# Performance work log

Measured on AMD Instinct MI355X. Metric: run time of the kernel, lower is better.

The kernel has to match this reference:

```python
import jax, jax.numpy as jnp
import numpy as np

RANK = 16
ALPHA = 32
SCALING = ALPHA / RANK  # 2.0


def setup_inputs() -> dict:
    key = jax.random.key(0)
    k1, k2, k3 = jax.random.split(key, 3)
    B_, S, D, O = 2, 4096, 4096, 4096
    x = jax.random.normal(k1, (B_, S, D), dtype=jnp.float32)
    # Dequantized base weight, torch Linear layout [out, in]
    W_base = jax.random.normal(k2, (O, D), dtype=jnp.float32) * 0.02
    # kaiming_uniform-ish init for lora_A [rank, in]
    bound = float(np.sqrt(6.0 / (1 + 5) / D))
    A = jax.random.uniform(k3, (RANK, D), dtype=jnp.float32, minval=-bound, maxval=bound)
    # lora_B initialized to zeros [out, rank]
    Bm = jnp.zeros((O, RANK), dtype=jnp.float32)
    return {"x": x, "W_base": W_base, "A": A, "B": Bm}


def reference(x, W_base, A, B):
    # Y = x @ W_base^T + (x @ A^T) @ B^T * scaling   (dropout p=0 -> identity)
    base_out = jnp.einsum('bsd,od->bso', x, W_base)
    lora_mid = jnp.einsum('bsd,rd->bsr', x, A)        # [B,S,rank]
    lora_out = jnp.einsum('bsr,or->bso', lora_mid, B) # [B,S,out]
    return base_out + lora_out * SCALING
```

## Files before the change

kernel.cpp:

```cpp
#include <hip/hip_runtime.h>
#include <hip/hip_bf16.h>

typedef __attribute__((ext_vector_type(8))) __bf16 bf16x8;
typedef __attribute__((ext_vector_type(4))) float  f32x4;

__global__ __launch_bounds__(256) void cvt_f32_bf16(
    const float* __restrict__ in, __bf16* __restrict__ out, long n8)
{
    long i = (long)blockIdx.x * blockDim.x + threadIdx.x;
    long stride = (long)gridDim.x * blockDim.x;
    for (; i < n8; i += stride) {
        const f32x4* p = (const f32x4*)(in + i * 8);
        f32x4 a = p[0], b = p[1];
        bf16x8 o;
        o[0] = (__bf16)a[0]; o[1] = (__bf16)a[1];
        o[2] = (__bf16)a[2]; o[3] = (__bf16)a[3];
        o[4] = (__bf16)b[0]; o[5] = (__bf16)b[1];
        o[6] = (__bf16)b[2]; o[7] = (__bf16)b[3];
        *(bf16x8*)(out + i * 8) = o;
    }
}

__global__ __launch_bounds__(256) void mid_and_cvt(
    const float* __restrict__ x, const float* __restrict__ A,
    float* __restrict__ mid, __bf16* __restrict__ Xb, int K, int M)
{
    int tid = threadIdx.x;
    int m0 = blockIdx.x * 4;

    float acc[4][16];
#pragma unroll
    for (int row = 0; row < 4; ++row)
#pragma unroll
        for (int r = 0; r < 16; ++r) acc[row][r] = 0.f;

    int iters = K / 2048;
    for (int it = 0; it < iters; ++it) {
        int k = it * 2048 + tid * 8;
        f32x4 xv[4][2];
#pragma unroll
        for (int row = 0; row < 4; ++row) {
            if (m0 + row < M) {
                const float* xr = x + (size_t)(m0 + row) * K;
                xv[row][0] = *(const f32x4*)(xr + k);
                xv[row][1] = *(const f32x4*)(xr + k + 4);
            } else {
                f32x4 z = {0.f,0.f,0.f,0.f};
                xv[row][0] = z; xv[row][1] = z;
            }
            if (Xb && m0 + row < M) {
                bf16x8 o;
                o[0] = (__bf16)xv[row][0][0]; o[1] = (__bf16)xv[row][0][1];
                o[2] = (__bf16)xv[row][0][2]; o[3] = (__bf16)xv[row][0][3];
                o[4] = (__bf16)xv[row][1][0]; o[5] = (__bf16)xv[row][1][1];
                o[6] = (__bf16)xv[row][1][2]; o[7] = (__bf16)xv[row][1][3];
                *(bf16x8*)(Xb + (size_t)(m0 + row) * K + k) = o;
            }
        }
#pragma unroll
        for (int r = 0; r < 16; ++r) {
            const f32x4* ap = (const f32x4*)(A + (size_t)r * K + k);
            f32x4 a0 = ap[0], a1 = ap[1];
#pragma unroll
            for (int row = 0; row < 4; ++row) {
                acc[row][r] += xv[row][0][0]*a0[0] + xv[row][0][1]*a0[1]
                             + xv[row][0][2]*a0[2] + xv[row][0][3]*a0[3]
                             + xv[row][1][0]*a1[0] + xv[row][1][1]*a1[1]
                             + xv[row][1][2]*a1[2] + xv[row][1][3]*a1[3];
            }
        }
    }

#pragma unroll
    for (int row = 0; row < 4; ++row)
#pragma unroll
        for (int r = 0; r < 16; ++r)
#pragma unroll
            for (int off = 32; off > 0; off >>= 1)
                acc[row][r] += __shfl_down(acc[row][r], off, 64);

    __shared__ float red[4][4][16];
    int lane = tid & 63, w = tid >> 6;
    if (lane == 0) {
#pragma unroll
        for (int row = 0; row < 4; ++row)
#pragma unroll
            for (int r = 0; r < 16; ++r) red[w][row][r] = acc[row][r];
    }
    __syncthreads();
    if (tid < 64) {
        int row = tid >> 4, r = tid & 15;
        if (m0 + row < M) {
            float s = red[0][row][r] + red[1][row][r]
                    + red[2][row][r] + red[3][row][r];
            mid[(size_t)(m0 + row) * 16 + r] = s;
        }
    }
}

#define GL16(g, l) __builtin_amdgcn_global_load_lds( \
    (const __attribute__((address_space(1))) void*)(g), \
    (__attribute__((address_space(3))) void*)(l), 16, 0, 0)

__global__ __launch_bounds__(512, 2) void gemm256(
    const __bf16* __restrict__ Xb,
    const __bf16* __restrict__ Wb,
    const float*  __restrict__ mid,
    const float*  __restrict__ Bl,
    float* __restrict__ out,
    int M, int N, int K)
{
    __shared__ __bf16 As[4][256 * 32];
    __shared__ __bf16 Bs[4][256 * 32];

    const int NT = K >> 5;

    int nbx = N >> 8, nby = M >> 8, nwg = nbx * nby;
    int bid = blockIdx.x, swz = bid;
    if ((nwg & 7) == 0) { int cpx = nwg >> 3; swz = (bid & 7) * cpx + (bid >> 3); }
    int by = swz / nbx, bx = swz % nbx;
    int m0 = by << 8, n0 = bx << 8;

    int tid = threadIdx.x;
    int lane = tid & 63;
    int w = tid >> 6;
    int wm = w >> 2, wn = w & 3;

    int q0 = tid >> 2;
    int c0 = tid & 3;
    int csrc = c0 ^ ((q0 >> 1) & 3);
    const __bf16* sA0 = Xb + (size_t)(m0 + q0) * K + csrc * 8;
    const __bf16* sA1 = sA0 + (size_t)128 * K;
    const __bf16* sB0 = Wb + (size_t)(n0 + q0) * K + csrc * 8;
    const __bf16* sB1 = sB0 + (size_t)128 * K;
    unsigned ldsw = (unsigned)w * 1024;

    int chunkSwz = (lane >> 4) ^ ((lane >> 1) & 3);
    unsigned aoff = (unsigned)((wm * 128 + (lane & 15)) * 64 + chunkSwz * 16);
    unsigned boff = (unsigned)((wn * 64  + (lane & 15)) * 64 + chunkSwz * 16);

    f32x4 acc[8][4];
    {
        int kh = lane >> 4;
        bf16x8 bI[4];
#pragma unroll
        for (int j = 0; j < 4; ++j) {
            bf16x8 v = {};
            if (kh < 2) {
                int col = n0 + wn * 64 + j * 16 + (lane & 15);
                const f32x4* p = (const f32x4*)(Bl + (size_t)col * 16 + kh * 8);
                f32x4 v0 = p[0], v1 = p[1];
                v[0] = (__bf16)(2.0f * v0[0]); v[1] = (__bf16)(2.0f * v0[1]);
                v[2] = (__bf16)(2.0f * v0[2]); v[3] = (__bf16)(2.0f * v0[3]);
                v[4] = (__bf16)(2.0f * v1[0]); v[5] = (__bf16)(2.0f * v1[1]);
                v[6] = (__bf16)(2.0f * v1[2]); v[7] = (__bf16)(2.0f * v1[3]);
            }
            bI[j] = v;
        }
#pragma unroll
        for (int i = 0; i < 8; ++i) {
            bf16x8 aI = {};
            if (kh < 2) {
                int row = m0 + wm * 128 + i * 16 + (lane & 15);
                const f32x4* p = (const f32x4*)(mid + (size_t)row * 16 + kh * 8);
                f32x4 v0 = p[0], v1 = p[1];
                aI[0] = (__bf16)v0[0]; aI[1] = (__bf16)v0[1];
                aI[2] = (__bf16)v0[2]; aI[3] = (__bf16)v0[3];
                aI[4] = (__bf16)v1[0]; aI[5] = (__bf16)v1[1];
                aI[6] = (__bf16)v1[2]; aI[7] = (__bf16)v1[3];
            }
            f32x4 z = {0.f, 0.f, 0.f, 0.f};
#pragma unroll
            for (int j = 0; j < 4; ++j)
                acc[i][j] = __builtin_amdgcn_mfma_f32_16x16x32_bf16(aI, bI[j], z, 0, 0, 0);
        }
    }

    GL16(sA0, (char*)As[0] + ldsw);
    GL16(sA1, (char*)As[0] + 8192 + ldsw);
    GL16(sB0, (char*)Bs[0] + ldsw);
    GL16(sB1, (char*)Bs[0] + 8192 + ldsw);
    GL16(sA0 + 32, (char*)As[1] + ldsw);
    GL16(sA1 + 32, (char*)As[1] + 8192 + ldsw);
    GL16(sB0 + 32, (char*)Bs[1] + ldsw);
    GL16(sB1 + 32, (char*)Bs[1] + 8192 + ldsw);
    asm volatile("s_waitcnt vmcnt(4)" ::: "memory");
    asm volatile("s_barrier" ::: "memory");

    int cur = 0;
    for (int t = 0; t < NT; ++t) {
        const __bf16* bufA = As[cur];
        const __bf16* bufB = Bs[cur];
        bool pf = (t + 2) < NT;
        int pb = (t + 2) & 3;
        size_t koff = (size_t)(t + 2) * 32;

        if (pf) {
            GL16(sA0 + koff, (char*)As[pb] + ldsw);
            GL16(sA1 + koff, (char*)As[pb] + 8192 + ldsw);
            GL16(sB0 + koff, (char*)Bs[pb] + ldsw);
            GL16(sB1 + koff, (char*)Bs[pb] + 8192 + ldsw);
        }

        bf16x8 bfr[4], af[8];
#pragma unroll
        for (int j = 0; j < 4; ++j)
            bfr[j] = *(const bf16x8*)((const char*)bufB + boff + j * 1024u);
#pragma unroll
        for (int i = 0; i < 8; ++i)
            af[i] = *(const bf16x8*)((const char*)bufA + aoff + i * 1024u);

        __builtin_amdgcn_s_setprio(1);
#pragma unroll
        for (int i = 0; i < 8; ++i)
#pragma unroll
            for (int j = 0; j < 4; ++j)
                acc[i][j] = __builtin_amdgcn_mfma_f32_16x16x32_bf16(
                    af[i], bfr[j], acc[i][j], 0, 0, 0);
        __builtin_amdgcn_s_setprio(0);

        if (pf) asm volatile("s_waitcnt vmcnt(4)" ::: "memory");
        else    asm volatile("s_waitcnt vmcnt(0)" ::: "memory");
        asm volatile("s_barrier" ::: "memory");

        cur = (cur + 1) & 3;
    }

#pragma unroll
    for (int i = 0; i < 8; ++i) {
        int rbase = m0 + wm * 128 + i * 16 + ((lane >> 4) << 2);
#pragma unroll
        for (int q = 0; q < 4; ++q) {
            float* orow = out + (size_t)(rbase + q) * N;
            int colb = n0 + wn * 64 + (lane & 15);
            orow[colb]      = acc[i][0][q];
            orow[colb + 16] = acc[i][1][q];
            orow[colb + 32] = acc[i][2][q];
            orow[colb + 48] = acc[i][3][q];
        }
    }
}

__global__ __launch_bounds__(256) void gemm_fb(
    const float* __restrict__ X, const float* __restrict__ W,
    const float* __restrict__ mid, const float* __restrict__ Bl,
    float* __restrict__ out, int M, int N, int K)
{
    __shared__ float As[64][16];
    __shared__ float Bs[64][16];
    int nbx = N / 64;
    int bx = blockIdx.x % nbx, by = blockIdx.x / nbx;
    int m0 = by * 64, n0 = bx * 64;
    int tid = threadIdx.x;
    int tr = tid >> 4, tc = tid & 15;

    float acc[4][4] = {};
    for (int kt = 0; kt < K; kt += 16) {
#pragma unroll
        for (int s = 0; s < 4; ++s) {
            int c = s * 256 + tid;
            int row = c >> 4, kk = c & 15;
            As[row][kk] = X[(size_t)(m0 + row) * K + kt + kk];
            Bs[row][kk] = W[(size_t)(n0 + row) * K + kt + kk];
        }
        __syncthreads();
#pragma unroll
        for (int kk = 0; kk < 16; ++kk) {
            float av[4], bv[4];
#pragma unroll
            for (int i = 0; i < 4; ++i) { av[i] = As[tr*4+i][kk]; bv[i] = Bs[tc*4+i][kk]; }
#pragma unroll
            for (int i = 0; i < 4; ++i)
#pragma unroll
                for (int j = 0; j < 4; ++j) acc[i][j] += av[i] * bv[j];
        }
        __syncthreads();
    }
#pragma unroll
    for (int i = 0; i < 4; ++i) {
        int row = m0 + tr * 4 + i;
#pragma unroll
        for (int j = 0; j < 4; ++j) {
            int col = n0 + tc * 4 + j;
            float s = 0.f;
#pragma unroll
            for (int r = 0; r < 16; ++r)
                s += mid[(size_t)row * 16 + r] * Bl[(size_t)col * 16 + r];
            out[(size_t)row * N + col] = acc[i][j] + 2.0f * s;
        }
    }
}

extern "C" void kernel_launch(void* const* d_in, const int* in_sizes, int n_in,
                              void* d_out, int out_size, void* d_ws, size_t ws_size,
                              hipStream_t stream)
{
    const float* x   = (const float*)d_in[0];
    const float* Wf  = (const float*)d_in[1];
    const float* A   = (const float*)d_in[2];
    const float* Bl  = (const float*)d_in[3];
    float* out = (float*)d_out;

    int D = in_sizes[2] / 16;
    int O = in_sizes[3] / 16;
    long M = (long)in_sizes[0] / D;
    int K = D, N = O;

    size_t xb_bytes  = (size_t)M * K * 2;
    size_t wb_bytes  = (size_t)N * K * 2;
    size_t mid_bytes = (size_t)M * 16 * 4;

    bool shapes_ok = (M % 256 == 0) && (N % 256 == 0) && (K % 2048 == 0);

    int midgrid = (int)((M + 3) / 4);

    if (shapes_ok && ws_size >= xb_bytes + wb_bytes + mid_bytes) {
        __bf16* Xb  = (__bf16*)d_ws;
        __bf16* Wbb = (__bf16*)((char*)d_ws + xb_bytes);
        float*  mid = (float*)((char*)d_ws + xb_bytes + wb_bytes);

        cvt_f32_bf16<<<2048, 256, 0, stream>>>(Wf, Wbb, (long)N * K / 8);
        mid_and_cvt<<<midgrid, 256, 0, stream>>>(x, A, mid, Xb, K, (int)M);
        int nwg = (int)(M / 256) * (N / 256);
        gemm256<<<nwg, 512, 0, stream>>>(Xb, Wbb, mid, Bl, out, (int)M, N, K);
    } else {
        float* mid = (float*)d_ws;
        mid_and_cvt<<<midgrid, 256, 0, stream>>>(x, A, mid, nullptr, K, (int)M);
        int nwg = (int)(M / 64) * (N / 64);
        gemm_fb<<<nwg, 256, 0, stream>>>(x, Wf, mid, Bl, out, (int)M, N, K);
    }
}
```

Before: 405.9 us.

## Merge preprocessing kernels and rewrite GEMM main loop with 32x32 MFMA ping-pong

```diff
diff --git a/kernel.cpp b/kernel.cpp
--- a/kernel.cpp
+++ b/kernel.cpp
@@ -1,39 +1,113 @@
 #include <hip/hip_runtime.h>
 #include <hip/hip_bf16.h>
 
-typedef __attribute__((ext_vector_type(8))) __bf16 bf16x8;
-typedef __attribute__((ext_vector_type(4))) float  f32x4;
-
-__global__ __launch_bounds__(256) void cvt_f32_bf16(
-    const float* __restrict__ in, __bf16* __restrict__ out, long n8)
+typedef __attribute__((ext_vector_type(8)))  __bf16 bf16x8;
+typedef __attribute__((ext_vector_type(4)))  float  f32x4;
+typedef __attribute__((ext_vector_type(16))) float  f32x16;
+
+__global__ __launch_bounds__(256) void preproc(
+    const float* __restrict__ x, const float* __restrict__ A,
+    const float* __restrict__ Wf,
+    float* __restrict__ mid, __bf16* __restrict__ Xb, __bf16* __restrict__ Wbb,
+    int K, int M, long nW8, int wBlocks)
 {
-    long i = (long)blockIdx.x * blockDim.x + threadIdx.x;
-    long stride = (long)gridDim.x * blockDim.x;
-    for (; i < n8; i += stride) {
-        const f32x4* p = (const f32x4*)(in + i * 8);
-        f32x4 a = p[0], b = p[1];
-        bf16x8 o;
-        o[0] = (__bf16)a[0]; o[1] = (__bf16)a[1];
-        o[2] = (__bf16)a[2]; o[3] = (__bf16)a[3];
-        o[4] = (__bf16)b[0]; o[5] = (__bf16)b[1];
-        o[6] = (__bf16)b[2]; o[7] = (__bf16)b[3];
-        *(bf16x8*)(out + i * 8) = o;
+    int tid = threadIdx.x;
+    if ((int)blockIdx.x < wBlocks) {
+        long i = (long)blockIdx.x * 256 + tid;
+        long stride = (long)wBlocks * 256;
+        for (; i < nW8; i += stride) {
+            const f32x4* p = (const f32x4*)(Wf + i * 8);
+            f32x4 a = p[0], b = p[1];
+            bf16x8 o;
+            o[0] = (__bf16)a[0]; o[1] = (__bf16)a[1];
+            o[2] = (__bf16)a[2]; o[3] = (__bf16)a[3];
+            o[4] = (__bf16)b[0]; o[5] = (__bf16)b[1];
+            o[6] = (__bf16)b[2]; o[7] = (__bf16)b[3];
+            *(bf16x8*)(Wbb + i * 8) = o;
+        }
+        return;
+    }
+
+    int m0 = ((int)blockIdx.x - wBlocks) * 4;
+    float acc[4][16];
+#pragma unroll
+    for (int row = 0; row < 4; ++row)
+#pragma unroll
+        for (int r = 0; r < 16; ++r) acc[row][r] = 0.f;
+
+    int iters = K / 2048;
+    for (int it = 0; it < iters; ++it) {
+        int k = it * 2048 + tid * 8;
+        f32x4 xv[4][2];
+#pragma unroll
+        for (int row = 0; row < 4; ++row) {
+            if (m0 + row < M) {
+                const float* xr = x + (size_t)(m0 + row) * K;
+                xv[row][0] = *(const f32x4*)(xr + k);
+                xv[row][1] = *(const f32x4*)(xr + k + 4);
+                bf16x8 o;
+                o[0] = (__bf16)xv[row][0][0]; o[1] = (__bf16)xv[row][0][1];
+                o[2] = (__bf16)xv[row][0][2]; o[3] = (__bf16)xv[row][0][3];
+                o[4] = (__bf16)xv[row][1][0]; o[5] = (__bf16)xv[row][1][1];
+                o[6] = (__bf16)xv[row][1][2]; o[7] = (__bf16)xv[row][1][3];
+                *(bf16x8*)(Xb + (size_t)(m0 + row) * K + k) = o;
+            } else {
+                f32x4 z = {0.f,0.f,0.f,0.f};
+                xv[row][0] = z; xv[row][1] = z;
+            }
+        }
+#pragma unroll
+        for (int r = 0; r < 16; ++r) {
+            const f32x4* ap = (const f32x4*)(A + (size_t)r * K + k);
+            f32x4 a0 = ap[0], a1 = ap[1];
+#pragma unroll
+            for (int row = 0; row < 4; ++row) {
+                acc[row][r] += xv[row][0][0]*a0[0] + xv[row][0][1]*a0[1]
+                             + xv[row][0][2]*a0[2] + xv[row][0][3]*a0[3]
+                             + xv[row][1][0]*a1[0] + xv[row][1][1]*a1[1]
+                             + xv[row][1][2]*a1[2] + xv[row][1][3]*a1[3];
+            }
+        }
+    }
+
+#pragma unroll
+    for (int row = 0; row < 4; ++row)
+#pragma unroll
+        for (int r = 0; r < 16; ++r)
+#pragma unroll
+            for (int off = 32; off > 0; off >>= 1)
+                acc[row][r] += __shfl_down(acc[row][r], off, 64);
+
+    __shared__ float red[4][4][16];
+    int lane = tid & 63, w = tid >> 6;
+    if (lane == 0) {
+#pragma unroll
+        for (int row = 0; row < 4; ++row)
+#pragma unroll
+            for (int r = 0; r < 16; ++r) red[w][row][r] = acc[row][r];
+    }
+    __syncthreads();
+    if (tid < 64) {
+        int row = tid >> 4, r = tid & 15;
+        if (m0 + row < M) {
+            float s = red[0][row][r] + red[1][row][r]
+                    + red[2][row][r] + red[3][row][r];
+            mid[(size_t)(m0 + row) * 16 + r] = s;
+        }
     }
 }
 
-__global__ __launch_bounds__(256) void mid_and_cvt(
+__global__ __launch_bounds__(256) void mid_only(
     const float* __restrict__ x, const float* __restrict__ A,
-    float* __restrict__ mid, __bf16* __restrict__ Xb, int K, int M)
+    float* __restrict__ mid, int K, int M)
 {
     int tid = threadIdx.x;
     int m0 = blockIdx.x * 4;
-
     float acc[4][16];
 #pragma unroll
     for (int row = 0; row < 4; ++row)
 #pragma unroll
         for (int r = 0; r < 16; ++r) acc[row][r] = 0.f;
-
     int iters = K / 2048;
     for (int it = 0; it < iters; ++it) {
         int k = it * 2048 + tid * 8;
@@ -48,14 +122,6 @@
                 f32x4 z = {0.f,0.f,0.f,0.f};
                 xv[row][0] = z; xv[row][1] = z;
             }
-            if (Xb && m0 + row < M) {
-                bf16x8 o;
-                o[0] = (__bf16)xv[row][0][0]; o[1] = (__bf16)xv[row][0][1];
-                o[2] = (__bf16)xv[row][0][2]; o[3] = (__bf16)xv[row][0][3];
-                o[4] = (__bf16)xv[row][1][0]; o[5] = (__bf16)xv[row][1][1];
-                o[6] = (__bf16)xv[row][1][2]; o[7] = (__bf16)xv[row][1][3];
-                *(bf16x8*)(Xb + (size_t)(m0 + row) * K + k) = o;
-            }
         }
 #pragma unroll
         for (int r = 0; r < 16; ++r) {
@@ -70,7 +136,6 @@
             }
         }
     }
-
 #pragma unroll
     for (int row = 0; row < 4; ++row)
 #pragma unroll
@@ -78,7 +143,6 @@
 #pragma unroll
             for (int off = 32; off > 0; off >>= 1)
                 acc[row][r] += __shfl_down(acc[row][r], off, 64);
-
     __shared__ float red[4][4][16];
     int lane = tid & 63, w = tid >> 6;
     if (lane == 0) {
@@ -101,6 +165,14 @@
 #define GL16(g, l) __builtin_amdgcn_global_load_lds( \
     (const __attribute__((address_space(1))) void*)(g), \
     (__attribute__((address_space(3))) void*)(l), 16, 0, 0)
+
+#define DSR(dst, addr, IMM) \
+    asm volatile("ds_read_b128 %0, %1 offset:" IMM : "=v"(dst) : "v"(addr))
+
+#define BAR()   __builtin_amdgcn_s_barrier()
+#define LGKM0() asm volatile("s_waitcnt lgkmcnt(0)" ::: )
+#define SCHED() __builtin_amdgcn_sched_barrier(0)
+#define MFMA32(d, a, b) d = __builtin_amdgcn_mfma_f32_32x32x16_bf16(a, b, d, 0, 0, 0)
 
 __global__ __launch_bounds__(512, 2) void gemm256(
     const __bf16* __restrict__ Xb,
@@ -135,110 +207,175 @@
     const __bf16* sB1 = sB0 + (size_t)128 * K;
     unsigned ldsw = (unsigned)w * 1024;
 
-    int chunkSwz = (lane >> 4) ^ ((lane >> 1) & 3);
-    unsigned aoff = (unsigned)((wm * 128 + (lane & 15)) * 64 + chunkSwz * 16);
-    unsigned boff = (unsigned)((wn * 64  + (lane & 15)) * 64 + chunkSwz * 16);
-
-    f32x4 acc[8][4];
+#define STAGE_A(t, b) do { size_t ko = (size_t)(t) * 32; \
+    GL16(sA0 + ko, (char*)As[b] + ldsw); \
+    GL16(sA1 + ko, (char*)As[b] + 8192 + ldsw); } while (0)
+#define STAGE_B(t, b) do { size_t ko = (size_t)(t) * 32; \
+    GL16(sB0 + ko, (char*)Bs[b] + ldsw); \
+    GL16(sB1 + ko, (char*)Bs[b] + 8192 + ldsw); } while (0)
+
+    int rmask = (lane >> 1) & 3;
+    unsigned a_base = (unsigned)((wm * 128 + (lane & 31)) * 64
+                                 + (((lane >> 5) ^ rmask) << 4));
+    unsigned b_base = (unsigned)((wn * 64 + (lane & 31)) * 64
+                                 + (((lane >> 5) ^ rmask) << 4));
+    unsigned a_addr = (unsigned)(size_t)(__attribute__((address_space(3))) __bf16*)&As[0][0] + a_base;
+    unsigned b_addr = (unsigned)(size_t)(__attribute__((address_space(3))) __bf16*)&Bs[0][0] + b_base;
+    unsigned a_addrX = a_addr ^ 32;
+    unsigned b_addrX = b_addr ^ 32;
+
+    f32x16 acc00, acc01, acc10, acc11, acc20, acc21, acc30, acc31;
     {
-        int kh = lane >> 4;
-        bf16x8 bI[4];
-#pragma unroll
-        for (int j = 0; j < 4; ++j) {
-            bf16x8 v = {};
-            if (kh < 2) {
-                int col = n0 + wn * 64 + j * 16 + (lane & 15);
-                const f32x4* p = (const f32x4*)(Bl + (size_t)col * 16 + kh * 8);
-                f32x4 v0 = p[0], v1 = p[1];
-                v[0] = (__bf16)(2.0f * v0[0]); v[1] = (__bf16)(2.0f * v0[1]);
-                v[2] = (__bf16)(2.0f * v0[2]); v[3] = (__bf16)(2.0f * v0[3]);
-                v[4] = (__bf16)(2.0f * v1[0]); v[5] = (__bf16)(2.0f * v1[1]);
-                v[6] = (__bf16)(2.0f * v1[2]); v[7] = (__bf16)(2.0f * v1[3]);
-            }
+        int ko = (lane >> 5) * 8;
+        bf16x8 bI[2];
+#pragma unroll
+        for (int j = 0; j < 2; ++j) {
+            int col = n0 + wn * 64 + j * 32 + (lane & 31);
+            const f32x4* p = (const f32x4*)(Bl + (size_t)col * 16 + ko);
+            f32x4 v0 = p[0], v1 = p[1];
+            bf16x8 v;
+            v[0] = (__bf16)(2.0f * v0[0]); v[1] = (__bf16)(2.0f * v0[1]);
+            v[2] = (__bf16)(2.0f * v0[2]); v[3] = (__bf16)(2.0f * v0[3]);
+            v[4] = (__bf16)(2.0f * v1[0]); v[5] = (__bf16)(2.0f * v1[1]);
+            v[6] = (__bf16)(2.0f * v1[2]); v[7] = (__bf16)(2.0f * v1[3]);
             bI[j] = v;
         }
-#pragma unroll
-        for (int i = 0; i < 8; ++i) {
-            bf16x8 aI = {};
-            if (kh < 2) {
-                int row = m0 + wm * 128 + i * 16 + (lane & 15);
-                const f32x4* p = (const f32x4*)(mid + (size_t)row * 16 + kh * 8);
-                f32x4 v0 = p[0], v1 = p[1];
-                aI[0] = (__bf16)v0[0]; aI[1] = (__bf16)v0[1];
-                aI[2] = (__bf16)v0[2]; aI[3] = (__bf16)v0[3];
-                aI[4] = (__bf16)v1[0]; aI[5] = (__bf16)v1[1];
-                aI[6] = (__bf16)v1[2]; aI[7] = (__bf16)v1[3];
-            }
-            f32x4 z = {0.f, 0.f, 0.f, 0.f};
-#pragma unroll
-            for (int j = 0; j < 4; ++j)
-                acc[i][j] = __builtin_amdgcn_mfma_f32_16x16x32_bf16(aI, bI[j], z, 0, 0, 0);
-        }
-    }
-
-    GL16(sA0, (char*)As[0] + ldsw);
-    GL16(sA1, (char*)As[0] + 8192 + ldsw);
-    GL16(sB0, (char*)Bs[0] + ldsw);
-    GL16(sB1, (char*)Bs[0] + 8192 + ldsw);
-    GL16(sA0 + 32, (char*)As[1] + ldsw);
-    GL16(sA1 + 32, (char*)As[1] + 8192 + ldsw);
-    GL16(sB0 + 32, (char*)Bs[1] + ldsw);
-    GL16(sB1 + 32, (char*)Bs[1] + 8192 + ldsw);
+        bf16x8 aI[4];
+#pragma unroll
+        for (int i = 0; i < 4; ++i) {
+            int row = m0 + wm * 128 + i * 32 + (lane & 31);
+            const f32x4* p = (const f32x4*)(mid + (size_t)row * 16 + ko);
+            f32x4 v0 = p[0], v1 = p[1];
+            bf16x8 v;
+            v[0] = (__bf16)v0[0]; v[1] = (__bf16)v0[1];
+            v[2] = (__bf16)v0[2]; v[3] = (__bf16)v0[3];
+            v[4] = (__bf16)v1[0]; v[5] = (__bf16)v1[1];
+            v[6] = (__bf16)v1[2]; v[7] = (__bf16)v1[3];
+            aI[i] = v;
+        }
+        f32x16 z = {};
+        acc00 = __builtin_amdgcn_mfma_f32_32x32x16_bf16(aI[0], bI[0], z, 0, 0, 0);
+        acc01 = __builtin_amdgcn_mfma_f32_32x32x16_bf16(aI[0], bI[1], z, 0, 0, 0);
+        acc10 = __builtin_amdgcn_mfma_f32_32x32x16_bf16(aI[1], bI[0], z, 0, 0, 0);
+        acc11 = __builtin_amdgcn_mfma_f32_32x32x16_bf16(aI[1], bI[1], z, 0, 0, 0);
+        acc20 = __builtin_amdgcn_mfma_f32_32x32x16_bf16(aI[2], bI[0], z, 0, 0, 0);
+        acc21 = __builtin_amdgcn_mfma_f32_32x32x16_bf16(aI[2], bI[1], z, 0, 0, 0);
+        acc30 = __builtin_amdgcn_mfma_f32_32x32x16_bf16(aI[3], bI[0], z, 0, 0, 0);
+        acc31 = __builtin_amdgcn_mfma_f32_32x32x16_bf16(aI[3], bI[1], z, 0, 0, 0);
+    }
+
+    STAGE_A(0, 0); STAGE_B(0, 0);
+    STAGE_A(1, 1); STAGE_B(1, 1);
     asm volatile("s_waitcnt vmcnt(4)" ::: "memory");
-    asm volatile("s_barrier" ::: "memory");
-
-    int cur = 0;
-    for (int t = 0; t < NT; ++t) {
-        const __bf16* bufA = As[cur];
-        const __bf16* bufB = Bs[cur];
-        bool pf = (t + 2) < NT;
-        int pb = (t + 2) & 3;
-        size_t koff = (size_t)(t + 2) * 32;
-
-        if (pf) {
-            GL16(sA0 + koff, (char*)As[pb] + ldsw);
-            GL16(sA1 + koff, (char*)As[pb] + 8192 + ldsw);
-            GL16(sB0 + koff, (char*)Bs[pb] + ldsw);
-            GL16(sB1 + koff, (char*)Bs[pb] + 8192 + ldsw);
-        }
-
-        bf16x8 bfr[4], af[8];
-#pragma unroll
-        for (int j = 0; j < 4; ++j)
-            bfr[j] = *(const bf16x8*)((const char*)bufB + boff + j * 1024u);
-#pragma unroll
-        for (int i = 0; i < 8; ++i)
-            af[i] = *(const bf16x8*)((const char*)bufA + aoff + i * 1024u);
-
+    BAR();
+
+    bf16x8 aX0k0, aX0k1, aX1k0, aX1k1, bX0k0, bX0k1, bX1k0, bX1k1;
+    bf16x8 aY0k0, aY0k1, aY1k0, aY1k1, bY0k0, bY0k1, bY1k0, bY1k1;
+    bf16x8 aH2k0, aH2k1, aH3k0, aH3k1, aJ2k0, aJ2k1, aJ3k0, aJ3k1;
+
+    DSR(aX0k0, a_addr,  "0");    DSR(aX0k1, a_addrX, "0");
+    DSR(aX1k0, a_addr,  "2048"); DSR(aX1k1, a_addrX, "2048");
+    DSR(bX0k0, b_addr,  "0");    DSR(bX0k1, b_addrX, "0");
+    DSR(bX1k0, b_addr,  "2048"); DSR(bX1k1, b_addrX, "2048");
+
+    for (int t = 0; t < NT; t += 2) {
+        unsigned o0 = (unsigned)(t & 3) << 14;
+        unsigned o1 = (unsigned)((t + 1) & 3) << 14;
+        unsigned o2 = (unsigned)((t + 2) & 3) << 14;
+        unsigned aT0 = a_addr + o0, aT0x = a_addrX + o0;
+        unsigned aT1 = a_addr + o1, aT1x = a_addrX + o1;
+        unsigned bT1 = b_addr + o1, bT1x = b_addrX + o1;
+        unsigned aT2 = a_addr + o2, aT2x = a_addrX + o2;
+        unsigned bT2 = b_addr + o2, bT2x = b_addrX + o2;
+        bool p2 = (t + 2) < NT;
+        bool p3 = (t + 3) < NT;
+
+        if (p2) STAGE_A(t + 2, (t + 2) & 3);
+        BAR();
+        LGKM0();
+        SCHED();
+        DSR(aH2k0, aT0,  "4096"); DSR(aH2k1, aT0x, "4096");
+        DSR(aH3k0, aT0,  "6144"); DSR(aH3k1, aT0x, "6144");
+        SCHED();
         __builtin_amdgcn_s_setprio(1);
-#pragma unroll
-        for (int i = 0; i < 8; ++i)
-#pragma unroll
-            for (int j = 0; j < 4; ++j)
-                acc[i][j] = __builtin_amdgcn_mfma_f32_16x16x32_bf16(
-                    af[i], bfr[j], acc[i][j], 0, 0, 0);
+        MFMA32(acc00, aX0k0, bX0k0); MFMA32(acc01, aX0k0, bX1k0);
+        MFMA32(acc10, aX1k0, bX0k0); MFMA32(acc11, aX1k0, bX1k0);
+        MFMA32(acc00, aX0k1, bX0k1); MFMA32(acc01, aX0k1, bX1k1);
+        MFMA32(acc10, aX1k1, bX0k1); MFMA32(acc11, aX1k1, bX1k1);
         __builtin_amdgcn_s_setprio(0);
 
-        if (pf) asm volatile("s_waitcnt vmcnt(4)" ::: "memory");
-        else    asm volatile("s_waitcnt vmcnt(0)" ::: "memory");
-        asm volatile("s_barrier" ::: "memory");
-
-        cur = (cur + 1) & 3;
-    }
-
-#pragma unroll
-    for (int i = 0; i < 8; ++i) {
-        int rbase = m0 + wm * 128 + i * 16 + ((lane >> 4) << 2);
-#pragma unroll
-        for (int q = 0; q < 4; ++q) {
-            float* orow = out + (size_t)(rbase + q) * N;
-            int colb = n0 + wn * 64 + (lane & 15);
-            orow[colb]      = acc[i][0][q];
-            orow[colb + 16] = acc[i][1][q];
-            orow[colb + 32] = acc[i][2][q];
-            orow[colb + 48] = acc[i][3][q];
-        }
-    }
+        if (p2) {
+            STAGE_B(t + 2, (t + 2) & 3);
+            asm volatile("s_waitcnt vmcnt(4)" ::: "memory");
+        } else {
+            asm volatile("s_waitcnt vmcnt(0)" ::: "memory");
+        }
+        BAR();
+        LGKM0();
+        SCHED();
+        DSR(aY0k0, aT1,  "0");    DSR(aY0k1, aT1x, "0");
+        DSR(aY1k0, aT1,  "2048"); DSR(aY1k1, aT1x, "2048");
+        DSR(bY0k0, bT1,  "0");    DSR(bY0k1, bT1x, "0");
+        DSR(bY1k0, bT1,  "2048"); DSR(bY1k1, bT1x, "2048");
+        SCHED();
+        __builtin_amdgcn_s_setprio(1);
+        MFMA32(acc20, aH2k0, bX0k0); MFMA32(acc21, aH2k0, bX1k0);
+        MFMA32(acc30, aH3k0, bX0k0); MFMA32(acc31, aH3k0, bX1k0);
+        MFMA32(acc20, aH2k1, bX0k1); MFMA32(acc21, aH2k1, bX1k1);
+        MFMA32(acc30, aH3k1, bX0k1); MFMA32(acc31, aH3k1, bX1k1);
+        __builtin_amdgcn_s_setprio(0);
+
+        if (p3) STAGE_A(t + 3, (t + 3) & 3);
+        BAR();
+        LGKM0();
+        SCHED();
+        DSR(aJ2k0, aT1,  "4096"); DSR(aJ2k1, aT1x, "4096");
+        DSR(aJ3k0, aT1,  "6144"); DSR(aJ3k1, aT1x, "6144");
+        SCHED();
+        __builtin_amdgcn_s_setprio(1);
+        MFMA32(acc00, aY0k0, bY0k0); MFMA32(acc01, aY0k0, bY1k0);
+        MFMA32(acc10, aY1k0, bY0k0); MFMA32(acc11, aY1k0, bY1k0);
+        MFMA32(acc00, aY0k1, bY0k1); MFMA32(acc01, aY0k1, bY1k1);
+        MFMA32(acc10, aY1k1, bY0k1); MFMA32(acc11, aY1k1, bY1k1);
+        __builtin_amdgcn_s_setprio(0);
+
+        if (p3) {
+            STAGE_B(t + 3, (t + 3) & 3);
+            asm volatile("s_waitcnt vmcnt(4)" ::: "memory");
+        } else {
+            asm volatile("s_waitcnt vmcnt(0)" ::: "memory");
+        }
+        BAR();
+        LGKM0();
+        SCHED();
+        if (p2) {
+            DSR(aX0k0, aT2,  "0");    DSR(aX0k1, aT2x, "0");
+            DSR(aX1k0, aT2,  "2048"); DSR(aX1k1, aT2x, "2048");
+            DSR(bX0k0, bT2,  "0");    DSR(bX0k1, bT2x, "0");
+            DSR(bX1k0, bT2,  "2048"); DSR(bX1k1, bT2x, "2048");
+        }
+        SCHED();
+        __builtin_amdgcn_s_setprio(1);
+        MFMA32(acc20, aJ2k0, bY0k0); MFMA32(acc21, aJ2k0, bY1k0);
+        MFMA32(acc30, aJ3k0, bY0k0); MFMA32(acc31, aJ3k0, bY1k0);
+        MFMA32(acc20, aJ2k1, bY0k1); MFMA32(acc21, aJ2k1, bY1k1);
+        MFMA32(acc30, aJ3k1, bY0k1); MFMA32(acc31, aJ3k1, bY1k1);
+        __builtin_amdgcn_s_setprio(0);
+    }
+
+#define STORE_FRAG(ACC, I, J) do { \
+    int rb = m0 + wm * 128 + (I) * 32 + 4 * (lane >> 5); \
+    int cb = n0 + wn * 64 + (J) * 32 + (lane & 31); \
+    _Pragma("unroll") \
+    for (int r = 0; r < 16; ++r) { \
+        int row = rb + (r & 3) + 8 * (r >> 2); \
+        out[(size_t)row * N + cb] = (ACC)[r]; \
+    } } while (0)
+
+    STORE_FRAG(acc00, 0, 0); STORE_FRAG(acc01, 0, 1);
+    STORE_FRAG(acc10, 1, 0); STORE_FRAG(acc11, 1, 1);
+    STORE_FRAG(acc20, 2, 0); STORE_FRAG(acc21, 2, 1);
+    STORE_FRAG(acc30, 3, 0); STORE_FRAG(acc31, 3, 1);
 }
 
 __global__ __launch_bounds__(256) void gemm_fb(
@@ -312,20 +449,22 @@
 
     bool shapes_ok = (M % 256 == 0) && (N % 256 == 0) && (K % 2048 == 0);
 
-    int midgrid = (int)((M + 3) / 4);
+    int midBlocks = (int)((M + 3) / 4);
 
     if (shapes_ok && ws_size >= xb_bytes + wb_bytes + mid_bytes) {
         __bf16* Xb  = (__bf16*)d_ws;
         __bf16* Wbb = (__bf16*)((char*)d_ws + xb_bytes);
         float*  mid = (float*)((char*)d_ws + xb_bytes + wb_bytes);
 
-        cvt_f32_bf16<<<2048, 256, 0, stream>>>(Wf, Wbb, (long)N * K / 8);
-        mid_and_cvt<<<midgrid, 256, 0, stream>>>(x, A, mid, Xb, K, (int)M);
+        const int wBlocks = 1024;
+        long nW8 = (long)N * K / 8;
+        preproc<<<wBlocks + midBlocks, 256, 0, stream>>>(
+            x, A, Wf, mid, Xb, Wbb, K, (int)M, nW8, wBlocks);
         int nwg = (int)(M / 256) * (N / 256);
         gemm256<<<nwg, 512, 0, stream>>>(Xb, Wbb, mid, Bl, out, (int)M, N, K);
     } else {
         float* mid = (float*)d_ws;
-        mid_and_cvt<<<midgrid, 256, 0, stream>>>(x, A, mid, nullptr, K, (int)M);
+        mid_only<<<midBlocks, 256, 0, stream>>>(x, A, mid, K, (int)M);
         int nwg = (int)(M / 64) * (N / 64);
         gemm_fb<<<nwg, 256, 0, stream>>>(x, Wf, mid, Bl, out, (int)M, N, K);
     }
```

New measurement: 347.5 us. -14.4%, faster.
